# Kernel optimization log

Hardware: AMD Instinct MI355X
Metric: run time of the kernel (lower is better)

Reference implementation:

```python
import jax, jax.numpy as jnp
import numpy as np

N = 40000   # entities
R = 200     # relations
T = 250000  # train edges (one direction)
E = 2 * T + N  # fwd + reverse + self-loops
D0, D = 100, 200   # init_emb_size, embedding_dim (= gc1_emb_size)
C, K = 128, 5      # conv channels, kernel size
B = 2048           # query batch
EPS = 1e-5


def setup_inputs() -> dict:
    key = jax.random.key(0)
    ks = jax.random.split(key, 24)
    def nrm(k, shape, s=0.05):
        return jax.random.normal(k, shape, jnp.float32) * s
    def bnp(k, dim):  # [gamma, beta, running_mean, running_var] stacked -> [4, dim]
        g = 1.0 + nrm(k, (dim,))
        b = nrm(jax.random.fold_in(k, 1), (dim,))
        m = nrm(jax.random.fold_in(k, 2), (dim,))
        v = 1.0 + 0.1 * jax.random.uniform(jax.random.fold_in(k, 3), (dim,), jnp.float32)
        return jnp.stack([g, b, m, v])
    inp = dict(
        src=jax.random.randint(ks[0], (E,), 0, N),
        dst=jax.random.randint(ks[1], (E,), 0, N),
        all_edge_type=jax.random.randint(ks[2], (E,), 0, R + 1),
        e1=jax.random.randint(ks[3], (B, 1), 0, N),
        rel=jax.random.randint(ks[4], (B, 1), 0, R),
        entity_id=jnp.arange(N),
        emb_e_w=nrm(ks[5], (N, D0), 0.1).at[0].set(0.0),   # padding_idx=0
        emb_rel_w=nrm(ks[6], (R, D), 0.1).at[0].set(0.0),
        w2=nrm(ks[7], (D0, D)), b2=nrm(ks[8], (D,)),
        alpha2=nrm(ks[9], (R + 1, 1)).at[0].set(0.0),
        w3=nrm(ks[10], (D, D)), b3=nrm(ks[11], (D,)),
        alpha3=nrm(ks[12], (R + 1, 1)).at[0].set(0.0),
        bn3=bnp(ks[13], D), bn4=bnp(ks[14], D),
        bn0=bnp(ks[15], 2), bn1=bnp(ks[16], C), bn2=bnp(ks[17], D),
        conv_w=nrm(ks[18], (C, 2, K)), conv_b=nrm(ks[19], (C,)),
        fc_w=nrm(ks[20], (D, D * C), 0.01), fc_b=nrm(ks[21], (D,)),
    )
    return inp


def _bn(x, p):  # eval-mode BatchNorm1d over last dim; p: [4, dim]
    g, b, m, v = p[0], p[1], p[2], p[3]
    return g * (x - m) * jax.lax.rsqrt(v + EPS) + b


def _bn_ch(x, p):  # x: [B, C, L]; normalize over channel dim
    g, b, m, v = (p[i][None, :, None] for i in range(4))
    return g * (x - m) * jax.lax.rsqrt(v + EPS) + b


def _gcn(x, w, b, alpha, src, dst, alp_types, alp_types_t, n):
    feats = x @ w                                   # [N, out]
    alp = alpha[alp_types] + alpha[alp_types_t]     # [E, 1]
    out = jax.ops.segment_sum(feats[src] * alp, dst, num_segments=n)
    return out + b


def reference(src, dst, all_edge_type, e1, rel, entity_id,
              emb_e_w, emb_rel_w, w2, b2, alpha2, w3, b3, alpha3,
              bn3, bn4, bn0, bn1, bn2, conv_w, conv_b, fc_w, fc_b):
    n = entity_id.shape[0]
    t = (all_edge_type.shape[0] - n) // 2
    # transpose edge types: [reverse, forward, self-loops]
    types_t = jnp.concatenate([all_edge_type[t:2 * t], all_edge_type[:t], all_edge_type[2 * t:]])

    x = emb_e_w[entity_id]                                   # [N, D0]
    x = _gcn(x, w2, b2, alpha2, src, dst, all_edge_type, types_t, n)
    x = jnp.tanh(_bn(x, bn3))                                # dropout: eval -> identity
    x = _gcn(x, w3, b3, alpha3, src, dst, all_edge_type, types_t, n)
    x = jnp.tanh(_bn(x, bn4))                                # final_bn + final_act
    e_all = x                                                # [N, D]

    e1_emb = e_all[e1]                                       # [B, 1, D]
    rel_emb = emb_rel_w[rel]                                 # [B, 1, D]
    h = jnp.concatenate([e1_emb, rel_emb], axis=1)           # [B, 2, D]
    h = _bn_ch(h, bn0)
    h = jax.lax.conv_general_dilated(h, conv_w, (1,), [(K // 2, K // 2)],
                                     dimension_numbers=('NCH', 'OIH', 'NCH'))
    h = h + conv_b[None, :, None]                            # [B, C, D]
    h = jax.nn.relu(_bn_ch(h, bn1))
    h = h.reshape(h.shape[0], -1)                            # [B, C*D]
    h = h @ fc_w.T + fc_b                                    # [B, D]
    h = jax.nn.relu(_bn(h, bn2))
    return jax.nn.sigmoid(h @ e_all.T)                       # [B, N]
```

## Files before the change

### kernel.cpp

```cpp
#include <hip/hip_runtime.h>
#include <math.h>

#define NENT 40000
#define NTE  250000
#define NE   540000
#define DIM0 100
#define DIM  200
#define CCH  128
#define BQ   2048
#define FCK  25600
#define EPSB 1e-5f
#define KPAD 224
#define NSPLIT 32
#define KSEG 800

typedef float f32x4 __attribute__((ext_vector_type(4)));
typedef _Float16 h8 __attribute__((ext_vector_type(8)));
typedef _Float16 h4 __attribute__((ext_vector_type(4)));

#if defined(__has_builtin)
#if __has_builtin(__builtin_amdgcn_global_load_lds)
#define HAVE_GLL 1
#endif
#endif

__device__ __forceinline__ void gload_lds16(const void* g, void* l) {
#ifdef HAVE_GLL
    __builtin_amdgcn_global_load_lds((const __attribute__((address_space(1))) unsigned int*)g,
                                     (__attribute__((address_space(3))) unsigned int*)l, 16, 0, 0);
#else
    *(uint4*)l = *(const uint4*)g;
#endif
}

__global__ void k_hist(const int* __restrict__ dst, int* __restrict__ deg) {
    int e = blockIdx.x * 256 + threadIdx.x;
    if (e < NE) atomicAdd(&deg[dst[e]], 1);
}

__global__ __launch_bounds__(1024) void k_scan(const int* __restrict__ deg,
        int* __restrict__ rowptr, int* __restrict__ cursor) {
    __shared__ int sums[1024];
    int t = threadIdx.x;
    int base = t * 40;
    int local[40];
    int s = 0;
    #pragma unroll
    for (int i = 0; i < 40; i++) {
        int idx = base + i;
        int v = (idx < NENT) ? deg[idx] : 0;
        local[i] = s;
        s += v;
    }
    sums[t] = s;
    __syncthreads();
    #pragma unroll
    for (int off = 1; off < 1024; off <<= 1) {
        int add = (t >= off) ? sums[t - off] : 0;
        __syncthreads();
        sums[t] += add;
        __syncthreads();
    }
    int prefix = (t == 0) ? 0 : sums[t - 1];
    #pragma unroll
    for (int i = 0; i < 40; i++) {
        int idx = base + i;
        if (idx < NENT) {
            int p = prefix + local[i];
            rowptr[idx] = p;
            cursor[idx] = p;
        }
    }
    if (t == 1023) rowptr[NENT] = prefix + s;
}

__global__ void k_scatter(const int* __restrict__ src, const int* __restrict__ dst,
                          const int* __restrict__ aet, const float* __restrict__ a2t,
                          const float* __restrict__ a3t, int* __restrict__ cursor,
                          int* __restrict__ ssrc, float* __restrict__ sa1,
                          float* __restrict__ sa2) {
    int e = blockIdx.x * 256 + threadIdx.x;
    if (e >= NE) return;
    int tt = (e < NTE) ? e + NTE : (e < 2 * NTE ? e - NTE : e);
    int t0 = aet[e], t1 = aet[tt];
    int pos = atomicAdd(&cursor[dst[e]], 1);
    ssrc[pos] = src[e];
    sa1[pos] = a2t[t0] + a2t[t1];
    sa2[pos] = a3t[t0] + a3t[t1];
}

template<bool W32>
__global__ __launch_bounds__(256) void k_agg_csr(const int* __restrict__ rowptr,
        const int* __restrict__ ssrc, const float* __restrict__ sa,
        const _Float16* __restrict__ feats, float* __restrict__ out32,
        const float* __restrict__ bias, const float* __restrict__ bn,
        _Float16* __restrict__ eh) {
    int w = threadIdx.x >> 6, l = threadIdx.x & 63;
    int row = blockIdx.x * 4 + w;
    int beg = rowptr[row], end = rowptr[row + 1];
    bool act = l < 50;
    int col = l * 4;
    float sx = 0.f, sy = 0.f, sz = 0.f, sw = 0.f;
    int i = beg;
    for (; i + 4 <= end; i += 4) {
        int i0 = ssrc[i], i1 = ssrc[i + 1], i2 = ssrc[i + 2], i3 = ssrc[i + 3];
        float a0 = sa[i], a1 = sa[i + 1], a2 = sa[i + 2], a3 = sa[i + 3];
        if (act) {
            h4 v0 = *(const h4*)(feats + (long)i0 * DIM + col);
            h4 v1 = *(const h4*)(feats + (long)i1 * DIM + col);
            h4 v2 = *(const h4*)(feats + (long)i2 * DIM + col);
            h4 v3 = *(const h4*)(feats + (long)i3 * DIM + col);
            sx += a0 * (float)v0[0] + a1 * (float)v1[0] + a2 * (float)v2[0] + a3 * (float)v3[0];
            sy += a0 * (float)v0[1] + a1 * (float)v1[1] + a2 * (float)v2[1] + a3 * (float)v3[1];
            sz += a0 * (float)v0[2] + a1 * (float)v1[2] + a2 * (float)v2[2] + a3 * (float)v3[2];
            sw += a0 * (float)v0[3] + a1 * (float)v1[3] + a2 * (float)v2[3] + a3 * (float)v3[3];
        }
    }
    for (; i < end; i++) {
        int i0 = ssrc[i];
        float a0 = sa[i];
        if (act) {
            h4 v0 = *(const h4*)(feats + (long)i0 * DIM + col);
            sx += a0 * (float)v0[0]; sy += a0 * (float)v0[1];
            sz += a0 * (float)v0[2]; sw += a0 * (float)v0[3];
        }
    }
    if (act) {
        float4 g  = *(const float4*)(bn + col);
        float4 be = *(const float4*)(bn + DIM + col);
        float4 m  = *(const float4*)(bn + 2 * DIM + col);
        float4 v  = *(const float4*)(bn + 3 * DIM + col);
        float4 bb = *(const float4*)(bias + col);
        float4 t;
        t.x = tanhf(g.x * (sx + bb.x - m.x) * rsqrtf(v.x + EPSB) + be.x);
        t.y = tanhf(g.y * (sy + bb.y - m.y) * rsqrtf(v.y + EPSB) + be.y);
        t.z = tanhf(g.z * (sz + bb.z - m.z) * rsqrtf(v.z + EPSB) + be.z);
        t.w = tanhf(g.w * (sw + bb.w - m.w) * rsqrtf(v.w + EPSB) + be.w);
        if (W32) *(float4*)(out32 + (long)row * DIM + col) = t;
        h4 e4 = { (_Float16)t.x, (_Float16)t.y, (_Float16)t.z, (_Float16)t.w };
        *(h4*)(eh + (long)row * KPAD + col) = e4;
    } else if (l < 56) {
        h4 z = { (_Float16)0.f, (_Float16)0.f, (_Float16)0.f, (_Float16)0.f };
        *(h4*)(eh + (long)row * KPAD + col) = z;
    }
}

__global__ void k_pack_emb(const float* __restrict__ emb, const int* __restrict__ ent,
                           _Float16* __restrict__ o) {
    long i = (long)blockIdx.x * 256 + threadIdx.x;
    if (i >= (long)NENT * 16) return;
    long m = i >> 4;
    int k0 = (int)(i & 15) << 3;
    h8 h = {};
    const float* p = emb + (long)ent[m] * DIM0 + k0;
    #pragma unroll
    for (int j = 0; j < 8; j++)
        if (k0 + j < DIM0) h[j] = (_Float16)p[j];
    *(h8*)(o + m * 128 + k0) = h;
}

__global__ void k_pack_B16(const float* __restrict__ w, _Float16* __restrict__ bf,
                           int kin, int kpad) {
    int i = blockIdx.x * 256 + threadIdx.x;
    if (i >= 208 * kpad) return;
    int k = i % kpad, n = i / kpad;
    bf[i] = (k < kin && n < DIM) ? (_Float16)w[(long)k * DIM + n] : (_Float16)0.f;
}

__global__ void k_hq(const int* __restrict__ e1, const int* __restrict__ rel,
                     const float* __restrict__ eall, const float* __restrict__ embrel,
                     const float* __restrict__ bn0, float* __restrict__ hq) {
    int i = blockIdx.x * 256 + threadIdx.x;
    if (i >= BQ * 2 * DIM) return;
    int d = i % DIM, c = (i / DIM) & 1, b = i / (2 * DIM);
    float val = (c == 0) ? eall[(long)e1[b] * DIM + d]
                         : embrel[(long)rel[b] * DIM + d];
    float g = bn0[c], be = bn0[2 + c], m = bn0[4 + c], v = bn0[6 + c];
    hq[i] = g * (val - m) * rsqrtf(v + EPSB) + be;
}

__global__ void k_pack_fcw(const float* __restrict__ w, _Float16* __restrict__ wf) {
    long i = (long)blockIdx.x * 256 + threadIdx.x;
    if (i >= (long)208 * (FCK / 8)) return;
    int n = (int)(i / (FCK / 8));
    long k0 = (i % (FCK / 8)) * 8;
    h8 h = {};
    if (n < DIM) {
        const float* p = w + (long)n * FCK + k0;
        #pragma unroll
        for (int j = 0; j < 8; j++) h[j] = (_Float16)p[j];
    }
    *(h8*)(wf + (long)n * FCK + k0) = h;
}

__global__ __launch_bounds__(256) void k_gemm16(
        const _Float16* __restrict__ A, const _Float16* __restrict__ B,
        _Float16* __restrict__ C, int kpad) {
    int w = threadIdx.x >> 6, l = threadIdx.x & 63;
    long m0 = (long)blockIdx.x * 64 + w * 16;
    long arow = m0 + (l & 15);
    int kg = (l >> 4) * 8;
    const _Float16* ap = A + arow * kpad + kg;
    f32x4 acc[13];
    #pragma unroll
    for (int i = 0; i < 13; i++) acc[i] = (f32x4){0.f, 0.f, 0.f, 0.f};
    for (int kb = 0; kb < kpad; kb += 32) {
        h8 a = *(const h8*)(ap + kb);
        #pragma unroll
        for (int nt = 0; nt < 13; nt++) {
            h8 b = *(const h8*)(B + (long)(nt * 16 + (l & 15)) * kpad + kb + kg);
            acc[nt] = __builtin_amdgcn_mfma_f32_16x16x32_f16(a, b, acc[nt], 0, 0, 0);
        }
    }
    long rowo = m0 + (l >> 4) * 4;
    #pragma unroll
    for (int nt = 0; nt < 13; nt++) {
        int col = nt * 16 + (l & 15);
        if (col < DIM) {
            #pragma unroll
            for (int rr = 0; rr < 4; rr++)
                C[(rowo + rr) * DIM + col] = (_Float16)acc[nt][rr];
        }
    }
}

__global__ __launch_bounds__(256) void k_conv2(const float* __restrict__ hq,
        const float* __restrict__ convw, const float* __restrict__ convb,
        const float* __restrict__ bn1, _Float16* __restrict__ hc) {
    __shared__ float hql[400];
    __shared__ float cwl[1280];
    __shared__ float scs[128], shs[128];
    int bl = blockIdx.x;
    int t = threadIdx.x;
    long b = bl;
    for (int i = t; i < 400; i += 256) hql[i] = hq[b * 400 + i];
    for (int i = t; i < 1280; i += 256) cwl[i] = convw[i];
    if (t < 128) {
        float g = bn1[t], be = bn1[CCH + t], m = bn1[2 * CCH + t], v = bn1[3 * CCH + t];
        float s = g * rsqrtf(v + EPSB);
        scs[t] = s;
        shs[t] = be - m * s + s * convb[t];
    }
    __syncthreads();
    int c = t >> 1, half = t & 1, p0 = half * 100;
    float cw[10];
    #pragma unroll
    for (int k = 0; k < 10; k++) cw[k] = cwl[c * 10 + k];
    float sc_ = scs[c], sh_ = shs[c];
    long obase = (long)bl * FCK + c * DIM + p0;
    for (int pc = 0; pc < 100; pc += 4) {
        float w0[8], w1[8];
        #pragma unroll
        for (int j = 0; j < 8; j++) {
            int pp = p0 + pc - 2 + j;
            bool ok = (pp >= 0 && pp < DIM);
            w0[j] = ok ? hql[pp] : 0.f;
            w1[j] = ok ? hql[DIM + pp] : 0.f;
        }
        h4 o;
        #pragma unroll
        for (int j = 0; j < 4; j++) {
            float s = 0.f;
            #pragma unroll
            for (int k = 0; k < 5; k++) s += w0[j + k] * cw[k] + w1[j + k] * cw[5 + k];
            o[j] = (_Float16)fmaxf(sc_ * s + sh_, 0.f);
        }
        *(h4*)&hc[obase + pc] = o;
    }
}

__global__ __launch_bounds__(256) void k_fc2(
        const _Float16* __restrict__ A, const _Float16* __restrict__ B,
        float* __restrict__ fcsum) {
    __shared__ __align__(16) _Float16 ldsB[2][6656];
    int bid = blockIdx.y * 8 + blockIdx.x;
    int wsw = (bid & 7) * 128 + (bid >> 3);
    int mb = wsw & 31, split = wsw >> 5;
    int t = threadIdx.x;
    int w = t >> 6, l = t & 63;
    int kbase = split * KSEG;
    long arow = mb * 64 + w * 16 + (l & 15);
    int kg = (l >> 4) * 8;
    const _Float16* ahp = A + arow * FCK + kbase + kg;

    #pragma unroll
    for (int i = 0; i < 4; i++) {
        int u = i * 256 + t;
        if (u < 832) {
            int r = u >> 2, kc = u & 3;
            gload_lds16(B + (long)r * FCK + kbase + kc * 8, &ldsB[0][u * 8]);
        }
    }
    h8 aN = *(const h8*)(ahp);

    f32x4 acc[13];
    #pragma unroll
    for (int i = 0; i < 13; i++) acc[i] = (f32x4){0.f, 0.f, 0.f, 0.f};

    int buf = 0;
    for (int ks = 0; ks < 25; ks++) {
        __syncthreads();
        if (ks + 1 < 25) {
            int knext = kbase + (ks + 1) * 32;
            #pragma unroll
            for (int i = 0; i < 4; i++) {
                int u = i * 256 + t;
                if (u < 832) {
                    int r = u >> 2, kc = u & 3;
                    gload_lds16(B + (long)r * FCK + knext + kc * 8, &ldsB[buf ^ 1][u * 8]);
                }
            }
        }
        h8 aC = aN;
        if (ks + 1 < 25) aN = *(const h8*)(ahp + (ks + 1) * 32);
        const _Float16* b_base = &ldsB[buf][(l & 15) * 32 + kg];
        #pragma unroll
        for (int nt = 0; nt < 13; nt++) {
            h8 b = *(const h8*)(b_base + nt * 512);
            acc[nt] = __builtin_amdgcn_mfma_f32_16x16x32_f16(aC, b, acc[nt], 0, 0, 0);
        }
        buf ^= 1;
    }
    long rowo = mb * 64 + w * 16 + (l >> 4) * 4;
    #pragma unroll
    for (int nt = 0; nt < 13; nt++) {
        int col = nt * 16 + (l & 15);
        if (col < DIM) {
            #pragma unroll
            for (int rr = 0; rr < 4; rr++)
                unsafeAtomicAdd(&fcsum[(rowo + rr) * DIM + col], acc[nt][rr]);
        }
    }
}

__global__ void k_fcreduce(const float* __restrict__ fcsum, const float* __restrict__ fcb,
                           const float* __restrict__ bn2, _Float16* __restrict__ h3) {
    int i = blockIdx.x * 256 + threadIdx.x;
    if (i >= BQ * KPAD) return;
    int j = i % KPAD, b = i / KPAD;
    _Float16 o = (_Float16)0.f;
    if (j < DIM) {
        float s = fcsum[(long)b * DIM + j] + fcb[j];
        float g = bn2[j], be = bn2[DIM + j], m = bn2[2 * DIM + j], v = bn2[3 * DIM + j];
        s = g * (s - m) * rsqrtf(v + EPSB) + be;
        o = (_Float16)fmaxf(s, 0.f);
    }
    h3[i] = o;
}

__global__ __launch_bounds__(256) void k_mfma_final(
        const _Float16* __restrict__ A, const _Float16* __restrict__ B,
        float* __restrict__ out) {
    __shared__ float tl[4][32][68];
    int bid = blockIdx.y * 8 + blockIdx.x;
    int wsw = (bid & 7) * 625 + (bid >> 3);
    int mbb = wsw & 7, nbb = wsw >> 3;
    int w = threadIdx.x >> 6, l = threadIdx.x & 63;
    int n0 = nbb * 64;
    int m0 = mbb * 256 + w * 64;
    int lr = l & 15;
    int kb = (l >> 4) * 8;
    const _Float16* aph = A + (long)(m0 + lr) * KPAD + kb;
    const _Float16* bph = B + (long)(n0 + lr) * KPAD + kb;
    h8 ac[4], bc[4], an[4], bn_[4];
    #pragma unroll
    for (int x = 0; x < 4; x++) {
        ac[x] = *(const h8*)(aph + (long)x * 16 * KPAD);
        bc[x] = *(const h8*)(bph + (long)x * 16 * KPAD);
    }
    f32x4 acc[4][4];
    #pragma unroll
    for (int i = 0; i < 4; i++)
        #pragma unroll
        for (int j = 0; j < 4; j++) acc[i][j] = (f32x4){0.f, 0.f, 0.f, 0.f};
    for (int kt = 0; kt < 7; kt++) {
        int ko = kt * 32 + 32;
        if (kt < 6) {
            #pragma unroll
            for (int x = 0; x < 4; x++) {
                an[x]  = *(const h8*)(aph + (long)x * 16 * KPAD + ko);
                bn_[x] = *(const h8*)(bph + (long)x * 16 * KPAD + ko);
            }
        }
        #pragma unroll
        for (int mt = 0; mt < 4; mt++)
            #pragma unroll
            for (int nt = 0; nt < 4; nt++)
                acc[mt][nt] = __builtin_amdgcn_mfma_f32_16x16x32_f16(ac[mt], bc[nt], acc[mt][nt], 0, 0, 0);
        if (kt < 6) {
            #pragma unroll
            for (int x = 0; x < 4; x++) { ac[x] = an[x]; bc[x] = bn_[x]; }
        }
    }
    #pragma unroll
    for (int hh = 0; hh < 2; hh++) {
        #pragma unroll
        for (int mt2 = 0; mt2 < 2; mt2++) {
            int mt = hh * 2 + mt2;
            #pragma unroll
            for (int nt = 0; nt < 4; nt++)
                #pragma unroll
                for (int r = 0; r < 4; r++)
                    tl[w][mt2 * 16 + (l >> 4) * 4 + r][nt * 16 + lr] = acc[mt][nt][r];
        }
        #pragma unroll
        for (int i = 0; i < 8; i++) {
            int rr = i * 4 + (l >> 4);
            f32x4 v = *(const f32x4*)&tl[w][rr][lr * 4];
            f32x4 o;
            o.x = __builtin_amdgcn_rcpf(1.f + __expf(-v.x));
            o.y = __builtin_amdgcn_rcpf(1.f + __expf(-v.y));
            o.z = __builtin_amdgcn_rcpf(1.f + __expf(-v.z));
            o.w = __builtin_amdgcn_rcpf(1.f + __expf(-v.w));
            long row = m0 + hh * 32 + rr;
            __builtin_nontemporal_store(o, (f32x4*)&out[row * NENT + n0 + lr * 4]);
        }
    }
}

extern "C" void kernel_launch(void* const* d_in, const int* in_sizes, int n_in,
                              void* d_out, int out_size, void* d_ws, size_t ws_size,
                              hipStream_t stream) {
    (void)in_sizes; (void)n_in; (void)out_size; (void)ws_size;
    const int* src      = (const int*)d_in[0];
    const int* dst      = (const int*)d_in[1];
    const int* aet      = (const int*)d_in[2];
    const int* e1       = (const int*)d_in[3];
    const int* rel      = (const int*)d_in[4];
    const int* entity   = (const int*)d_in[5];
    const float* emb_e  = (const float*)d_in[6];
    const float* embrel = (const float*)d_in[7];
    const float* w2     = (const float*)d_in[8];
    const float* b2     = (const float*)d_in[9];
    const float* alpha2 = (const float*)d_in[10];
    const float* w3     = (const float*)d_in[11];
    const float* b3     = (const float*)d_in[12];
    const float* alpha3 = (const float*)d_in[13];
    const float* bn3    = (const float*)d_in[14];
    const float* bn4    = (const float*)d_in[15];
    const float* bn0    = (const float*)d_in[16];
    const float* bn1    = (const float*)d_in[17];
    const float* bn2    = (const float*)d_in[18];
    const float* convw  = (const float*)d_in[19];
    const float* convb  = (const float*)d_in[20];
    const float* fcw    = (const float*)d_in[21];
    const float* fcb    = (const float*)d_in[22];
    float* out = (float*)d_out;
    float* ws = (float*)d_ws;

    _Float16* feats_f = (_Float16*)ws;
    _Float16* fcw_f   = (_Float16*)(ws + 4500000);
    float* xbuf   = ws + 16000000;
    _Float16* emb16 = (_Float16*)(ws + 24000000);
    _Float16* x1_f  = (_Float16*)(ws + 29120000);
    _Float16* e_f   = (_Float16*)(ws + 29120000);
    int*   deg    = (int*)(ws + 38100000);
    int*   rowptr = (int*)(ws + 38150000);
    int*   cursor = (int*)(ws + 38200000);
    int*   ssrc   = (int*)(ws + 38250000);
    float* sa1    = ws + 38800000;
    float* sa2    = ws + 39350000;
    float* fcsum  = ws + 39900000;
    float* hq     = ws + 40350000;
    _Float16* h3_f = (_Float16*)(ws + 41200000);
    _Float16* w2t_f = (_Float16*)(ws + 41700000);
    _Float16* w3t_f = (_Float16*)(ws + 41740000);
    _Float16* hc_f  = (_Float16*)(ws + 43000000);

    hipMemsetAsync(deg, 0, NENT * 4, stream);
    k_hist<<<(NE + 255) / 256, 256, 0, stream>>>(dst, deg);
    k_scan<<<1, 1024, 0, stream>>>(deg, rowptr, cursor);
    k_scatter<<<(NE + 255) / 256, 256, 0, stream>>>(src, dst, aet, alpha2, alpha3,
                                                    cursor, ssrc, sa1, sa2);

    k_pack_emb<<<(NENT * 16 + 255) / 256, 256, 0, stream>>>(emb_e, entity, emb16);
    k_pack_B16<<<(208 * 128 + 255) / 256, 256, 0, stream>>>(w2, w2t_f, DIM0, 128);
    k_pack_B16<<<(208 * KPAD + 255) / 256, 256, 0, stream>>>(w3, w3t_f, DIM, KPAD);

    k_gemm16<<<NENT / 64, 256, 0, stream>>>(emb16, w2t_f, feats_f, 128);
    k_agg_csr<false><<<NENT / 4, 256, 0, stream>>>(rowptr, ssrc, sa1, feats_f,
                                                   nullptr, b2, bn3, x1_f);

    k_gemm16<<<NENT / 64, 256, 0, stream>>>(x1_f, w3t_f, feats_f, KPAD);
    k_agg_csr<true><<<NENT / 4, 256, 0, stream>>>(rowptr, ssrc, sa2, feats_f,
                                                  xbuf, b3, bn4, e_f);

    k_hq<<<(BQ * 2 * DIM + 255) / 256, 256, 0, stream>>>(e1, rel, xbuf, embrel, bn0, hq);
    k_pack_fcw<<<(int)(((long)208 * (FCK / 8) + 255) / 256), 256, 0, stream>>>(fcw, fcw_f);

    hipMemsetAsync(fcsum, 0, (size_t)BQ * DIM * 4, stream);
    k_conv2<<<BQ, 256, 0, stream>>>(hq, convw, convb, bn1, hc_f);
    k_fc2<<<dim3(8, 128), 256, 0, stream>>>(hc_f, fcw_f, fcsum);
    k_fcreduce<<<(BQ * KPAD + 255) / 256, 256, 0, stream>>>(fcsum, fcb, bn2, h3_f);

    k_mfma_final<<<dim3(8, NENT / 64), 256, 0, stream>>>(h3_f, e_f, out);
}
```

Measured before the change: 547.1 us.

## Aggregate before the GCN weight transform and fuse bias/BN/tanh into the GEMM epilogue

The order of each GCN layer is flipped from transform-then-aggregate to aggregate-then-transform, using the linearity of A(XW) = (AX)W. Layer 1 now gathers 100-wide fp16 embeddings (stride 104) instead of 200-wide features. This cuts the irregular gather traffic in the first aggregation. The bias, batchnorm and tanh move into the MFMA GEMM epilogue, and the fp32 e_all buffer is dropped, so k_hq reads the fp16 copy instead. The aggregated sums are rounded to fp16 before the GEMM, which adds a small precision risk.

```diff
diff --git a/kernel.cpp b/kernel.cpp
--- a/kernel.cpp
+++ b/kernel.cpp
@@ -11,6 +11,7 @@
 #define FCK  25600
 #define EPSB 1e-5f
 #define KPAD 224
+#define EMBS 104
 #define NSPLIT 32
 #define KSEG 800
 
@@ -89,16 +90,14 @@
     sa2[pos] = a3t[t0] + a3t[t1];
 }
 
-template<bool W32>
-__global__ __launch_bounds__(256) void k_agg_csr(const int* __restrict__ rowptr,
+template<int NL, int NPADL, int SS, int OS>
+__global__ __launch_bounds__(256) void k_agg_raw(const int* __restrict__ rowptr,
         const int* __restrict__ ssrc, const float* __restrict__ sa,
-        const _Float16* __restrict__ feats, float* __restrict__ out32,
-        const float* __restrict__ bias, const float* __restrict__ bn,
-        _Float16* __restrict__ eh) {
+        const _Float16* __restrict__ srcd, _Float16* __restrict__ outd) {
     int w = threadIdx.x >> 6, l = threadIdx.x & 63;
     int row = blockIdx.x * 4 + w;
     int beg = rowptr[row], end = rowptr[row + 1];
-    bool act = l < 50;
+    bool act = l < NL;
     int col = l * 4;
     float sx = 0.f, sy = 0.f, sz = 0.f, sw = 0.f;
     int i = beg;
@@ -106,10 +105,10 @@
         int i0 = ssrc[i], i1 = ssrc[i + 1], i2 = ssrc[i + 2], i3 = ssrc[i + 3];
         float a0 = sa[i], a1 = sa[i + 1], a2 = sa[i + 2], a3 = sa[i + 3];
         if (act) {
-            h4 v0 = *(const h4*)(feats + (long)i0 * DIM + col);
-            h4 v1 = *(const h4*)(feats + (long)i1 * DIM + col);
-            h4 v2 = *(const h4*)(feats + (long)i2 * DIM + col);
-            h4 v3 = *(const h4*)(feats + (long)i3 * DIM + col);
+            h4 v0 = *(const h4*)(srcd + (long)i0 * SS + col);
+            h4 v1 = *(const h4*)(srcd + (long)i1 * SS + col);
+            h4 v2 = *(const h4*)(srcd + (long)i2 * SS + col);
+            h4 v3 = *(const h4*)(srcd + (long)i3 * SS + col);
             sx += a0 * (float)v0[0] + a1 * (float)v1[0] + a2 * (float)v2[0] + a3 * (float)v3[0];
             sy += a0 * (float)v0[1] + a1 * (float)v1[1] + a2 * (float)v2[1] + a3 * (float)v3[1];
             sz += a0 * (float)v0[2] + a1 * (float)v1[2] + a2 * (float)v2[2] + a3 * (float)v3[2];
@@ -120,60 +119,49 @@
         int i0 = ssrc[i];
         float a0 = sa[i];
         if (act) {
-            h4 v0 = *(const h4*)(feats + (long)i0 * DIM + col);
+            h4 v0 = *(const h4*)(srcd + (long)i0 * SS + col);
             sx += a0 * (float)v0[0]; sy += a0 * (float)v0[1];
             sz += a0 * (float)v0[2]; sw += a0 * (float)v0[3];
         }
     }
     if (act) {
-        float4 g  = *(const float4*)(bn + col);
-        float4 be = *(const float4*)(bn + DIM + col);
-        float4 m  = *(const float4*)(bn + 2 * DIM + col);
-        float4 v  = *(const float4*)(bn + 3 * DIM + col);
-        float4 bb = *(const float4*)(bias + col);
-        float4 t;
-        t.x = tanhf(g.x * (sx + bb.x - m.x) * rsqrtf(v.x + EPSB) + be.x);
-        t.y = tanhf(g.y * (sy + bb.y - m.y) * rsqrtf(v.y + EPSB) + be.y);
-        t.z = tanhf(g.z * (sz + bb.z - m.z) * rsqrtf(v.z + EPSB) + be.z);
-        t.w = tanhf(g.w * (sw + bb.w - m.w) * rsqrtf(v.w + EPSB) + be.w);
-        if (W32) *(float4*)(out32 + (long)row * DIM + col) = t;
-        h4 e4 = { (_Float16)t.x, (_Float16)t.y, (_Float16)t.z, (_Float16)t.w };
-        *(h4*)(eh + (long)row * KPAD + col) = e4;
-    } else if (l < 56) {
+        h4 o = { (_Float16)sx, (_Float16)sy, (_Float16)sz, (_Float16)sw };
+        *(h4*)(outd + (long)row * OS + col) = o;
+    } else if (l < NPADL) {
         h4 z = { (_Float16)0.f, (_Float16)0.f, (_Float16)0.f, (_Float16)0.f };
-        *(h4*)(eh + (long)row * KPAD + col) = z;
+        *(h4*)(outd + (long)row * OS + col) = z;
     }
 }
 
 __global__ void k_pack_emb(const float* __restrict__ emb, const int* __restrict__ ent,
                            _Float16* __restrict__ o) {
     long i = (long)blockIdx.x * 256 + threadIdx.x;
-    if (i >= (long)NENT * 16) return;
-    long m = i >> 4;
-    int k0 = (int)(i & 15) << 3;
+    if (i >= (long)NENT * 13) return;
+    long m = i / 13;
+    int k0 = (int)(i % 13) * 8;
     h8 h = {};
     const float* p = emb + (long)ent[m] * DIM0 + k0;
     #pragma unroll
     for (int j = 0; j < 8; j++)
         if (k0 + j < DIM0) h[j] = (_Float16)p[j];
-    *(h8*)(o + m * 128 + k0) = h;
+    *(h8*)(o + m * EMBS + k0) = h;
 }
 
 __global__ void k_pack_B16(const float* __restrict__ w, _Float16* __restrict__ bf,
-                           int kin, int kpad) {
+                           int kin, int kpad, int nrows) {
     int i = blockIdx.x * 256 + threadIdx.x;
-    if (i >= 208 * kpad) return;
+    if (i >= nrows * kpad) return;
     int k = i % kpad, n = i / kpad;
     bf[i] = (k < kin && n < DIM) ? (_Float16)w[(long)k * DIM + n] : (_Float16)0.f;
 }
 
 __global__ void k_hq(const int* __restrict__ e1, const int* __restrict__ rel,
-                     const float* __restrict__ eall, const float* __restrict__ embrel,
+                     const _Float16* __restrict__ ef, const float* __restrict__ embrel,
                      const float* __restrict__ bn0, float* __restrict__ hq) {
     int i = blockIdx.x * 256 + threadIdx.x;
     if (i >= BQ * 2 * DIM) return;
     int d = i % DIM, c = (i / DIM) & 1, b = i / (2 * DIM);
-    float val = (c == 0) ? eall[(long)e1[b] * DIM + d]
+    float val = (c == 0) ? (float)ef[(long)e1[b] * KPAD + d]
                          : embrel[(long)rel[b] * DIM + d];
     float g = bn0[c], be = bn0[2 + c], m = bn0[4 + c], v = bn0[6 + c];
     hq[i] = g * (val - m) * rsqrtf(v + EPSB) + be;
@@ -193,33 +181,47 @@
     *(h8*)(wf + (long)n * FCK + k0) = h;
 }
 
-__global__ __launch_bounds__(256) void k_gemm16(
+template<int NT>
+__global__ __launch_bounds__(256) void k_gemm16f(
         const _Float16* __restrict__ A, const _Float16* __restrict__ B,
-        _Float16* __restrict__ C, int kpad) {
+        const float* __restrict__ bias, const float* __restrict__ bn,
+        _Float16* __restrict__ C, int kpad, int ostride) {
     int w = threadIdx.x >> 6, l = threadIdx.x & 63;
     long m0 = (long)blockIdx.x * 64 + w * 16;
     long arow = m0 + (l & 15);
     int kg = (l >> 4) * 8;
     const _Float16* ap = A + arow * kpad + kg;
-    f32x4 acc[13];
-    #pragma unroll
-    for (int i = 0; i < 13; i++) acc[i] = (f32x4){0.f, 0.f, 0.f, 0.f};
+    f32x4 acc[NT];
+    #pragma unroll
+    for (int i = 0; i < NT; i++) acc[i] = (f32x4){0.f, 0.f, 0.f, 0.f};
     for (int kb = 0; kb < kpad; kb += 32) {
         h8 a = *(const h8*)(ap + kb);
         #pragma unroll
-        for (int nt = 0; nt < 13; nt++) {
+        for (int nt = 0; nt < NT; nt++) {
             h8 b = *(const h8*)(B + (long)(nt * 16 + (l & 15)) * kpad + kb + kg);
             acc[nt] = __builtin_amdgcn_mfma_f32_16x16x32_f16(a, b, acc[nt], 0, 0, 0);
         }
     }
     long rowo = m0 + (l >> 4) * 4;
     #pragma unroll
-    for (int nt = 0; nt < 13; nt++) {
+    for (int nt = 0; nt < NT; nt++) {
         int col = nt * 16 + (l & 15);
-        if (col < DIM) {
+        if (col < ostride) {
+            _Float16 vals[4];
+            if (col < DIM) {
+                float g = bn[col], be = bn[DIM + col], m = bn[2 * DIM + col],
+                      v = bn[3 * DIM + col], bb = bias[col];
+                float sc = g * rsqrtf(v + EPSB);
+                #pragma unroll
+                for (int rr = 0; rr < 4; rr++)
+                    vals[rr] = (_Float16)tanhf(sc * (acc[nt][rr] + bb - m) + be);
+            } else {
+                #pragma unroll
+                for (int rr = 0; rr < 4; rr++) vals[rr] = (_Float16)0.f;
+            }
             #pragma unroll
             for (int rr = 0; rr < 4; rr++)
-                C[(rowo + rr) * DIM + col] = (_Float16)acc[nt][rr];
+                C[(rowo + rr) * ostride + col] = vals[rr];
         }
     }
 }
@@ -448,24 +450,24 @@
     float* out = (float*)d_out;
     float* ws = (float*)d_ws;
 
-    _Float16* feats_f = (_Float16*)ws;
-    _Float16* fcw_f   = (_Float16*)(ws + 4500000);
-    float* xbuf   = ws + 16000000;
-    _Float16* emb16 = (_Float16*)(ws + 24000000);
-    _Float16* x1_f  = (_Float16*)(ws + 29120000);
-    _Float16* e_f   = (_Float16*)(ws + 29120000);
-    int*   deg    = (int*)(ws + 38100000);
-    int*   rowptr = (int*)(ws + 38150000);
-    int*   cursor = (int*)(ws + 38200000);
-    int*   ssrc   = (int*)(ws + 38250000);
-    float* sa1    = ws + 38800000;
-    float* sa2    = ws + 39350000;
-    float* fcsum  = ws + 39900000;
-    float* hq     = ws + 40350000;
-    _Float16* h3_f = (_Float16*)(ws + 41200000);
-    _Float16* w2t_f = (_Float16*)(ws + 41700000);
-    _Float16* w3t_f = (_Float16*)(ws + 41740000);
-    _Float16* hc_f  = (_Float16*)(ws + 43000000);
+    _Float16* emb16 = (_Float16*)ws;
+    _Float16* aggE  = (_Float16*)(ws + 3000000);
+    _Float16* x1_f  = (_Float16*)(ws + 6000000);
+    _Float16* aggX  = (_Float16*)(ws + 11000000);
+    _Float16* e_f   = (_Float16*)(ws + 16000000);
+    _Float16* fcw_f = (_Float16*)(ws + 21000000);
+    _Float16* hc_f  = (_Float16*)(ws + 24000000);
+    int*   deg    = (int*)(ws + 51000000);
+    int*   rowptr = (int*)(ws + 51050000);
+    int*   cursor = (int*)(ws + 51100000);
+    int*   ssrc   = (int*)(ws + 51200000);
+    float* sa1    = ws + 51800000;
+    float* sa2    = ws + 52400000;
+    float* fcsum  = ws + 53000000;
+    float* hq     = ws + 53500000;
+    _Float16* h3_f  = (_Float16*)(ws + 54400000);
+    _Float16* w2t_f = (_Float16*)(ws + 54700000);
+    _Float16* w3t_f = (_Float16*)(ws + 54750000);
 
     hipMemsetAsync(deg, 0, NENT * 4, stream);
     k_hist<<<(NE + 255) / 256, 256, 0, stream>>>(dst, deg);
@@ -473,19 +475,19 @@
     k_scatter<<<(NE + 255) / 256, 256, 0, stream>>>(src, dst, aet, alpha2, alpha3,
                                                     cursor, ssrc, sa1, sa2);
 
-    k_pack_emb<<<(NENT * 16 + 255) / 256, 256, 0, stream>>>(emb_e, entity, emb16);
-    k_pack_B16<<<(208 * 128 + 255) / 256, 256, 0, stream>>>(w2, w2t_f, DIM0, 128);
-    k_pack_B16<<<(208 * KPAD + 255) / 256, 256, 0, stream>>>(w3, w3t_f, DIM, KPAD);
-
-    k_gemm16<<<NENT / 64, 256, 0, stream>>>(emb16, w2t_f, feats_f, 128);
-    k_agg_csr<false><<<NENT / 4, 256, 0, stream>>>(rowptr, ssrc, sa1, feats_f,
-                                                   nullptr, b2, bn3, x1_f);
-
-    k_gemm16<<<NENT / 64, 256, 0, stream>>>(x1_f, w3t_f, feats_f, KPAD);
-    k_agg_csr<true><<<NENT / 4, 256, 0, stream>>>(rowptr, ssrc, sa2, feats_f,
-                                                  xbuf, b3, bn4, e_f);
-
-    k_hq<<<(BQ * 2 * DIM + 255) / 256, 256, 0, stream>>>(e1, rel, xbuf, embrel, bn0, hq);
+    k_pack_emb<<<(NENT * 13 + 255) / 256, 256, 0, stream>>>(emb_e, entity, emb16);
+    k_pack_B16<<<(208 * 128 + 255) / 256, 256, 0, stream>>>(w2, w2t_f, DIM0, 128, 208);
+    k_pack_B16<<<(224 * KPAD + 255) / 256, 256, 0, stream>>>(w3, w3t_f, DIM, KPAD, 224);
+
+    k_agg_raw<26, 32, EMBS, 128><<<NENT / 4, 256, 0, stream>>>(rowptr, ssrc, sa1,
+                                                               emb16, aggE);
+    k_gemm16f<13><<<NENT / 64, 256, 0, stream>>>(aggE, w2t_f, b2, bn3, x1_f, 128, DIM);
+
+    k_agg_raw<50, 56, DIM, KPAD><<<NENT / 4, 256, 0, stream>>>(rowptr, ssrc, sa2,
+                                                               x1_f, aggX);
+    k_gemm16f<14><<<NENT / 64, 256, 0, stream>>>(aggX, w3t_f, b3, bn4, e_f, KPAD, KPAD);
+
+    k_hq<<<(BQ * 2 * DIM + 255) / 256, 256, 0, stream>>>(e1, rel, e_f, embrel, bn0, hq);
     k_pack_fcw<<<(int)(((long)208 * (FCK / 8) + 255) / 256), 256, 0, stream>>>(fcw, fcw_f);
 
     hipMemsetAsync(fcsum, 0, (size_t)BQ * DIM * 4, stream);
```

Measured after the change: 543.9 us. Within noise of the previous version (-0.6%).
